# Optimization experiments

Hardware: AMD Instinct MI355X
Metric: run time of the kernel (lower is better)

## Reference

```python
import jax, jax.numpy as jnp
import numpy as np

N_NODES = 100000
N_EDGES = 1600000
IN_CH = 128
HID = 64
N_CLASSES = 16
N_GRAPHS = 64


def setup_inputs() -> dict:
    key = jax.random.key(0)
    ks = jax.random.split(key, 10)
    x = jax.random.normal(ks[0], (N_NODES, IN_CH), dtype=jnp.float32)
    edge_index = jax.random.randint(ks[1], (2, N_EDGES), 0, N_NODES, dtype=jnp.int64)
    edge_weight = jax.random.uniform(ks[2], (N_EDGES,), dtype=jnp.float32)
    batch = jnp.sort(jax.random.randint(ks[3], (N_NODES,), 0, N_GRAPHS, dtype=jnp.int64))
    s1 = 1.0 / np.sqrt(IN_CH)
    s2 = 1.0 / np.sqrt(HID)
    W1 = jax.random.uniform(ks[4], (IN_CH, HID), jnp.float32, -s1, s1)
    b1 = jnp.zeros((HID,), jnp.float32)
    W2 = jax.random.uniform(ks[5], (HID, HID), jnp.float32, -s2, s2)
    b2 = jnp.zeros((HID,), jnp.float32)
    Wl = jax.random.uniform(ks[6], (HID, N_CLASSES), jnp.float32, -s2, s2)
    bl = jax.random.uniform(ks[7], (N_CLASSES,), jnp.float32, -s2, s2)
    return {"x": x, "edge_index": edge_index, "edge_weight": edge_weight,
            "batch": batch, "W1": W1, "b1": b1, "W2": W2, "b2": b2,
            "Wl": Wl, "bl": bl}


def _gcn_conv(x, src, dst, ew, W, b, n_nodes):
    # PyG GCNConv: h = x @ W; symmetric normalization with self-loops;
    # out[dst] += norm * h[src]; out += bias.
    deg = jax.ops.segment_sum(ew, dst, num_segments=n_nodes)
    deg_inv_sqrt = jnp.where(deg > 0, jax.lax.rsqrt(jnp.maximum(deg, 1e-30)), 0.0)
    norm = deg_inv_sqrt[src] * ew * deg_inv_sqrt[dst]  # [E']
    h = x @ W                                          # [N, out]
    msg = h[src] * norm[:, None]                       # [E', out] gather
    out = jax.ops.segment_sum(msg, dst, num_segments=n_nodes)  # scatter-add
    return out + b


def reference(x, edge_index, edge_weight, batch, W1, b1, W2, b2, Wl, bl):
    n = x.shape[0]
    # add self loops once (weight 1.0), shared by both conv layers
    loop = jnp.arange(n, dtype=edge_index.dtype)
    src = jnp.concatenate([edge_index[0], loop])
    dst = jnp.concatenate([edge_index[1], loop])
    ew = jnp.concatenate([edge_weight, jnp.ones((n,), edge_weight.dtype)])

    h = jax.nn.relu(_gcn_conv(x, src, dst, ew, W1, b1, n))
    h = jax.nn.relu(_gcn_conv(h, src, dst, ew, W2, b2, n))

    # global_mean_pool over graphs
    sums = jax.ops.segment_sum(h, batch, num_segments=N_GRAPHS)  # [G, HID]
    cnt = jax.ops.segment_sum(jnp.ones((n,), h.dtype), batch, num_segments=N_GRAPHS)
    pooled = sums / jnp.maximum(cnt, 1.0)[:, None]

    return pooled @ Wl + bl
```

## Files before the change

### kernel.cpp

```cpp
#include <hip/hip_runtime.h>
#include <hip/hip_fp16.h>

#define N_NODES   100000
#define N_EDGES   1600000
#define IN_CH     128
#define HID       64
#define N_CLASSES 16
#define N_GRAPHS  64

#define BK_SH     9
#define BK_NODES  512
#define NB        ((N_NODES + BK_NODES - 1) / BK_NODES)
#define BK_CAP    10240
#define CH_EDGES  4096
#define EPT       16
#define NCH       ((N_EDGES + CH_EDGES - 1) / CH_EDGES)
#define AGG_NPW   2

typedef __attribute__((ext_vector_type(8))) short bf16x8;
typedef __attribute__((ext_vector_type(4))) float f32x4;
typedef __attribute__((ext_vector_type(4))) unsigned u32x4;
typedef __attribute__((ext_vector_type(2))) unsigned u32x2;

__device__ __forceinline__ unsigned short f2bf(float f) {
    unsigned u = __float_as_uint(f);
    u += 0x7fffu + ((u >> 16) & 1u);
    return (unsigned short)(u >> 16);
}
__device__ __forceinline__ f32x4 bf4v(uint2 v) {
    u32x4 u;
    u.x = v.x << 16; u.y = v.x & 0xffff0000u;
    u.z = v.y << 16; u.w = v.y & 0xffff0000u;
    return __builtin_bit_cast(f32x4, u);
}
__device__ __forceinline__ float dec_ew(unsigned v) {
    return __half2float(__ushort_as_half((unsigned short)(v >> 17)));
}

#if __has_builtin(__builtin_amdgcn_make_buffer_rsrc) && \
    __has_builtin(__builtin_amdgcn_raw_buffer_load_b32) && \
    __has_builtin(__builtin_amdgcn_raw_buffer_load_b64)
struct BufView {
    __amdgpu_buffer_rsrc_t rsrc;
    __device__ __forceinline__ void init(const void* p) {
        rsrc = __builtin_amdgcn_make_buffer_rsrc((void*)p, (short)0,
                                                 (int)0xFFFFFFFF, 0x00020000);
    }
    __device__ __forceinline__ unsigned ld32(unsigned off) const {
        return __builtin_amdgcn_raw_buffer_load_b32(rsrc, (int)off, 0, 0);
    }
    __device__ __forceinline__ uint2 ld64(unsigned off) const {
        u32x2 r = __builtin_amdgcn_raw_buffer_load_b64(rsrc, (int)off, 0, 0);
        return make_uint2(r.x, r.y);
    }
};
#else
struct BufView {
    const char* base;
    __device__ __forceinline__ void init(const void* p) { base = (const char*)p; }
    __device__ __forceinline__ unsigned ld32(unsigned off) const {
        return *(const unsigned*)(base + off);
    }
    __device__ __forceinline__ uint2 ld64(unsigned off) const {
        return *(const uint2*)(base + off);
    }
};
#endif

__global__ void k_init(int* __restrict__ bcursor, float* __restrict__ pooled) {
    int i = blockIdx.x * 256 + threadIdx.x;
    if (i < NB) bcursor[i] = i * BK_CAP;
    if (i < N_GRAPHS * HID) pooled[i] = 0.0f;
}

__global__ void k_binscatter(const int* __restrict__ src, const int* __restrict__ dst,
                             const float* __restrict__ ew, int* __restrict__ bcursor,
                             int2* __restrict__ bedges) {
    __shared__ int  hist[NB];
    __shared__ int  offs[NB];
    __shared__ int  gbase[NB];
    __shared__ int  sc[256];
    __shared__ int2 stage[CH_EDGES];
    __shared__ int  dest[CH_EDGES];
    const int t = threadIdx.x;
    const int base = blockIdx.x * CH_EDGES;
    const int nloc = min(CH_EDGES, N_EDGES - base);

    for (int i = t; i < NB; i += 256) hist[i] = 0;
    __syncthreads();

    int myb[EPT], myr[EPT], myp[EPT]; float myw[EPT];
#pragma unroll
    for (int j = 0; j < EPT; ++j) {
        int i = base + j * 256 + t;
        if (i < N_EDGES) {
            int s = src[i], d = dst[i];
            int b = d >> BK_SH;
            myb[j] = b;
            myr[j] = atomicAdd(&hist[b], 1);
            myp[j] = s | ((d & (BK_NODES - 1)) << 17);
            myw[j] = ew[i];
        } else {
            myb[j] = -1;
        }
    }
    __syncthreads();

    int v = (t < NB) ? hist[t] : 0;
    sc[t] = v;
    __syncthreads();
    for (int off = 1; off < 256; off <<= 1) {
        int a = (t >= off) ? sc[t - off] : 0;
        __syncthreads();
        sc[t] += a;
        __syncthreads();
    }
    if (t < NB) {
        offs[t] = sc[t] - v;
        gbase[t] = (v > 0) ? atomicAdd(&bcursor[t], v) : 0;
    }
    __syncthreads();

#pragma unroll
    for (int j = 0; j < EPT; ++j) {
        if (myb[j] >= 0) {
            int p = offs[myb[j]] + myr[j];
            stage[p] = make_int2(myp[j], __float_as_int(myw[j]));
            dest[p] = gbase[myb[j]] + myr[j];
        }
    }
    __syncthreads();

    for (int i = t; i < nloc; i += 256)
        bedges[dest[i]] = stage[i];
}

__global__ __launch_bounds__(256) void k_build(const int* __restrict__ bcursor,
                                               const int2* __restrict__ bedges,
                                               int2* __restrict__ rowse,
                                               float* __restrict__ dis,
                                               unsigned* __restrict__ csr) {
    __shared__ int2  eds[BK_CAP];
    __shared__ int   cnt[BK_NODES];
    __shared__ float dsum[BK_NODES];
    __shared__ int   cur[BK_NODES];
    __shared__ int   sc[256];
    const int b = blockIdx.x;
    const int t = threadIdx.x;
    const int beg = b * BK_CAP, end = bcursor[b];
    const int n = end - beg;

    for (int i = t; i < BK_NODES; i += 256) { cnt[i] = 0; dsum[i] = 0.0f; }
    __syncthreads();

    for (int i = t; i < n; i += 256) {
        int2 e = bedges[beg + i];
        eds[i] = e;
        int dl = ((unsigned)e.x) >> 17;
        atomicAdd(&cnt[dl], 1);
        atomicAdd(&dsum[dl], __int_as_float(e.y));
    }
    __syncthreads();

    int a0 = cnt[2 * t], a1 = cnt[2 * t + 1];
    int pair = a0 + a1;
    sc[t] = pair;
    __syncthreads();
    for (int off = 1; off < 256; off <<= 1) {
        int a = (t >= off) ? sc[t - off] : 0;
        __syncthreads();
        sc[t] += a;
        __syncthreads();
    }
    int excl = sc[t] - pair;
    cur[2 * t] = excl;
    cur[2 * t + 1] = excl + a0;
    {
        int n0 = b * BK_NODES + 2 * t;
        if (n0 < N_NODES) {
            rowse[n0] = make_int2(beg + excl, beg + excl + a0);
            dis[n0] = rsqrtf(1.0f + dsum[2 * t]);
        }
        int n1 = n0 + 1;
        if (n1 < N_NODES) {
            rowse[n1] = make_int2(beg + excl + a0, beg + excl + a0 + a1);
            dis[n1] = rsqrtf(1.0f + dsum[2 * t + 1]);
        }
    }
    __syncthreads();

    for (int i = t; i < n; i += 256) {
        int2 e = eds[i];
        int dl = ((unsigned)e.x) >> 17;
        int s = e.x & 0x1FFFF;
        unsigned short w16 = __half_as_ushort(__float2half(__int_as_float(e.y)));
        int pos = beg + atomicAdd(&cur[dl], 1);
        csr[pos] = (unsigned)s | ((unsigned)w16 << 17);
    }
}

template <int K, bool INB>
__global__ __launch_bounds__(256) void k_gemm(const float* __restrict__ x,
                                              const unsigned short* __restrict__ xb,
                                              const float* __restrict__ W,
                                              const float* __restrict__ dis,
                                              unsigned short* __restrict__ hb) {
    constexpr int AS = K + 8;
    __shared__ unsigned short wt[64 * AS];
    const int t    = threadIdx.x;
    const int lane = t & 63;
    const int wave = t >> 6;
    const int m    = lane & 15;
    const int quad = lane >> 4;
    const int rowbase = blockIdx.x * 64;

    bf16x8 afrag[K / 32];

    if constexpr (!INB) {
        __shared__ unsigned short a_s[64 * AS];
        constexpr int CPR = K / 8;
        for (int c = t; c < 64 * CPR; c += 256) {
            int row = c / CPR, cc = c % CPR;
            int gr = rowbase + row;
            float4 v0, v1;
            if (gr < N_NODES) {
                v0 = *(const float4*)&x[(long)gr * K + cc * 8];
                v1 = *(const float4*)&x[(long)gr * K + cc * 8 + 4];
            } else {
                v0 = make_float4(0.f, 0.f, 0.f, 0.f); v1 = v0;
            }
            uint4 p;
            p.x = f2bf(v0.x) | ((unsigned)f2bf(v0.y) << 16);
            p.y = f2bf(v0.z) | ((unsigned)f2bf(v0.w) << 16);
            p.z = f2bf(v1.x) | ((unsigned)f2bf(v1.y) << 16);
            p.w = f2bf(v1.z) | ((unsigned)f2bf(v1.w) << 16);
            *(uint4*)&a_s[row * AS + cc * 8] = p;
        }
        for (int idx = t; idx < K * 64; idx += 256) {
            int k = idx >> 6, n = idx & 63;
            wt[n * AS + k] = f2bf(W[idx]);
        }
        __syncthreads();
#pragma unroll
        for (int ks = 0; ks < K / 32; ++ks)
            afrag[ks] = *(const bf16x8*)&a_s[(wave * 16 + m) * AS + ks * 32 + quad * 8];
    } else {
        const int gr = rowbase + wave * 16 + m;
#pragma unroll
        for (int ks = 0; ks < K / 32; ++ks) {
            if (gr < N_NODES)
                afrag[ks] = *(const bf16x8*)&xb[(long)gr * K + ks * 32 + quad * 8];
            else
                afrag[ks] = (bf16x8){0, 0, 0, 0, 0, 0, 0, 0};
        }
        for (int idx = t; idx < K * 64; idx += 256) {
            int k = idx >> 6, n = idx & 63;
            wt[n * AS + k] = f2bf(W[idx]);
        }
        __syncthreads();
    }

    bf16x8 bfrag[4][K / 32];
#pragma unroll
    for (int nt = 0; nt < 4; ++nt)
#pragma unroll
        for (int ks = 0; ks < K / 32; ++ks)
            bfrag[nt][ks] = *(const bf16x8*)&wt[(nt * 16 + m) * AS + ks * 32 + quad * 8];

    f32x4 acc[4];
#pragma unroll
    for (int nt = 0; nt < 4; ++nt) acc[nt] = (f32x4){0.f, 0.f, 0.f, 0.f};

#pragma unroll
    for (int ks = 0; ks < K / 32; ++ks) {
#pragma unroll
        for (int nt = 0; nt < 4; ++nt)
            acc[nt] = __builtin_amdgcn_mfma_f32_16x16x32_bf16(afrag[ks], bfrag[nt][ks],
                                                              acc[nt], 0, 0, 0);
    }

#pragma unroll
    for (int i = 0; i < 4; ++i) {
        int gr = rowbase + wave * 16 + quad * 4 + i;
        if (gr < N_NODES) {
            float dsc = dis[gr];
#pragma unroll
            for (int nt = 0; nt < 4; ++nt)
                hb[(long)gr * HID + nt * 16 + m] = f2bf(dsc * acc[nt][i]);
        }
    }
}

#define NEXTBLK(pb_, eb_, jb_, hv_)                                           \
    do {                                                                      \
        if (p0 < e0)      { pb_ = p0; eb_ = e0; jb_ = 0; hv_ = true; p0 += 16; } \
        else if (p1 < e1) { pb_ = p1; eb_ = e1; jb_ = 1; hv_ = true; p1 += 16; } \
        else              { hv_ = false; }                                    \
    } while (0)

#define AGG_STEP(pC_, eC_, jC_, c0_, c1_, c2_, c3_, r0_, r1_, r2_, r3_, hC_,  \
                 n0_, n1_, n2_, n3_, s0_, s1_, s2_, s3_, hN_)                 \
    do {                                                                      \
        const float w0_ = (pC_ + g      < eC_) ? dec_ew(c0_) : 0.f;           \
        const float w1_ = (pC_ + 4 + g  < eC_) ? dec_ew(c1_) : 0.f;           \
        const float w2_ = (pC_ + 8 + g  < eC_) ? dec_ew(c2_) : 0.f;           \
        const float w3_ = (pC_ + 12 + g < eC_) ? dec_ew(c3_) : 0.f;           \
        const int jcur_ = jC_;                                                \
        if (hN_) {        \
            s0_ = vh.ld64(((n0_ & 0x1FFFF) << 7) | coff);                     \
            s1_ = vh.ld64(((n1_ & 0x1FFFF) << 7) | coff);                     \
            s2_ = vh.ld64(((n2_ & 0x1FFFF) << 7) | coff);                     \
            s3_ = vh.ld64(((n3_ & 0x1FFFF) << 7) | coff);                     \
        }                                                                     \
        NEXTBLK(pC_, eC_, jC_, hC_);    \
        if (hC_) {                                                            \
            const int last_ = eC_ - 1;                                        \
            c0_ = vc.ld32((unsigned)(min(pC_ + g,      last_) << 2));         \
            c1_ = vc.ld32((unsigned)(min(pC_ + 4 + g,  last_) << 2));         \
            c2_ = vc.ld32((unsigned)(min(pC_ + 8 + g,  last_) << 2));         \
            c3_ = vc.ld32((unsigned)(min(pC_ + 12 + g, last_) << 2));         \
        }                                                                     \
        f32x4 t_ = bf4v(r0_) * w0_;                                           \
        t_ += bf4v(r1_) * w1_;                                                \
        t_ += bf4v(r2_) * w2_;                                                \
        t_ += bf4v(r3_) * w3_;                                                \
        if (jcur_ == 0) acc0 += t_; else acc1 += t_;                          \
    } while (0)

template <bool OB>
__global__ __launch_bounds__(256) void k_aggregate(const int2* __restrict__ rowse,
                            const unsigned* __restrict__ csr,
                            const uint2* __restrict__ hb, const float* __restrict__ dis,
                            const float* __restrict__ b, const int* __restrict__ batch,
                            float* __restrict__ pooled, uint2* __restrict__ outb) {
    __shared__ float psh[4 * AGG_NPW][HID];
    const int tid  = threadIdx.x;
    const int lane = tid & 63;
    const int g    = lane >> 4;
    const int c4   = lane & 15;
    const int wave = tid >> 6;
    const int node0 = (blockIdx.x * 4 + wave) * AGG_NPW;
    const float4 bb = ((const float4*)b)[c4];
    const f32x4 bbv = {bb.x, bb.y, bb.z, bb.w};

    BufView vc; vc.init(csr);
    BufView vh; vh.init(hb);
    const unsigned coff = (unsigned)(c4 << 3);

    const int2 rs0 = rowse[node0];
    const int2 rs1 = rowse[node0 + 1];
    const uint2 hs0 = hb[node0 * 16 + c4];
    const uint2 hs1 = hb[(node0 + 1) * 16 + c4];
    const float dd0 = dis[node0];
    const float dd1 = dis[node0 + 1];

    f32x4 acc0 = (g == 0) ? bf4v(hs0) : (f32x4){0.f, 0.f, 0.f, 0.f};
    f32x4 acc1 = (g == 0) ? bf4v(hs1) : (f32x4){0.f, 0.f, 0.f, 0.f};

    int p0 = rs0.x, e0 = rs0.y, p1 = rs1.x, e1 = rs1.y;

    int pA = 0, eAn = 0, jA = 0; bool hA = false;
    int pB = 0, eBn = 0, jB = 0; bool hB = false;
    unsigned cA0 = 0, cA1 = 0, cA2 = 0, cA3 = 0;
    unsigned cB0 = 0, cB1 = 0, cB2 = 0, cB3 = 0;
    uint2 rA0 = {0, 0}, rA1 = {0, 0}, rA2 = {0, 0}, rA3 = {0, 0};
    uint2 rB0 = {0, 0}, rB1 = {0, 0}, rB2 = {0, 0}, rB3 = {0, 0};

    NEXTBLK(pA, eAn, jA, hA);
    if (hA) {
        const int last = eAn - 1;
        cA0 = vc.ld32((unsigned)(min(pA + g,      last) << 2));
        cA1 = vc.ld32((unsigned)(min(pA + 4 + g,  last) << 2));
        cA2 = vc.ld32((unsigned)(min(pA + 8 + g,  last) << 2));
        cA3 = vc.ld32((unsigned)(min(pA + 12 + g, last) << 2));
        NEXTBLK(pB, eBn, jB, hB);
        if (hB) {
            const int lastB = eBn - 1;
            cB0 = vc.ld32((unsigned)(min(pB + g,      lastB) << 2));
            cB1 = vc.ld32((unsigned)(min(pB + 4 + g,  lastB) << 2));
            cB2 = vc.ld32((unsigned)(min(pB + 8 + g,  lastB) << 2));
            cB3 = vc.ld32((unsigned)(min(pB + 12 + g, lastB) << 2));
        }
        rA0 = vh.ld64(((cA0 & 0x1FFFF) << 7) | coff);
        rA1 = vh.ld64(((cA1 & 0x1FFFF) << 7) | coff);
        rA2 = vh.ld64(((cA2 & 0x1FFFF) << 7) | coff);
        rA3 = vh.ld64(((cA3 & 0x1FFFF) << 7) | coff);
    }

    bool par = false;
    while (par ? hB : hA) {
        if (!par) {
            AGG_STEP(pA, eAn, jA, cA0, cA1, cA2, cA3, rA0, rA1, rA2, rA3, hA,
                     cB0, cB1, cB2, cB3, rB0, rB1, rB2, rB3, hB);
        } else {
            AGG_STEP(pB, eBn, jB, cB0, cB1, cB2, cB3, rB0, rB1, rB2, rB3, hB,
                     cA0, cA1, cA2, cA3, rA0, rA1, rA2, rA3, hA);
        }
        par = !par;
    }

#pragma unroll
    for (int i = 0; i < 4; ++i) {
        float t0 = acc0[i];
        t0 += __shfl_xor(t0, 16); t0 += __shfl_xor(t0, 32);
        acc0[i] = t0;
        float t1 = acc1[i];
        t1 += __shfl_xor(t1, 16); t1 += __shfl_xor(t1, 32);
        acc1[i] = t1;
    }

    if (g == 0) {
        f32x4 o0 = acc0 * dd0 + bbv;
        f32x4 o1 = acc1 * dd1 + bbv;
        o0.x = fmaxf(o0.x, 0.f); o0.y = fmaxf(o0.y, 0.f);
        o0.z = fmaxf(o0.z, 0.f); o0.w = fmaxf(o0.w, 0.f);
        o1.x = fmaxf(o1.x, 0.f); o1.y = fmaxf(o1.y, 0.f);
        o1.z = fmaxf(o1.z, 0.f); o1.w = fmaxf(o1.w, 0.f);
        if constexpr (OB) {
            uint2 pk0, pk1;
            pk0.x = (unsigned)f2bf(o0.x) | ((unsigned)f2bf(o0.y) << 16);
            pk0.y = (unsigned)f2bf(o0.z) | ((unsigned)f2bf(o0.w) << 16);
            pk1.x = (unsigned)f2bf(o1.x) | ((unsigned)f2bf(o1.y) << 16);
            pk1.y = (unsigned)f2bf(o1.z) | ((unsigned)f2bf(o1.w) << 16);
            outb[node0 * 16 + c4] = pk0;
            outb[(node0 + 1) * 16 + c4] = pk1;
        } else {
            *(f32x4*)&psh[wave * AGG_NPW][c4 * 4] = o0;
            *(f32x4*)&psh[wave * AGG_NPW + 1][c4 * 4] = o1;
        }
    }

    if constexpr (!OB) {
        __syncthreads();
        if (tid < HID) {
            const int nb0 = blockIdx.x * 4 * AGG_NPW;
            int curg = batch[nb0];
            float a = 0.f;
#pragma unroll
            for (int j = 0; j < 4 * AGG_NPW; ++j) {
                int bg = batch[nb0 + j];
                if (bg != curg) {
                    atomicAdd(&pooled[curg * HID + tid], a);
                    a = 0.f; curg = bg;
                }
                a += psh[j][tid];
            }
            atomicAdd(&pooled[curg * HID + tid], a);
        }
    }
}

__global__ __launch_bounds__(1024) void k_out(const float* __restrict__ pooled,
                      const int* __restrict__ batch,
                      const float* __restrict__ Wl, const float* __restrict__ bl,
                      float* __restrict__ out) {
    __shared__ int bnd[N_GRAPHS + 1];
    int tid = threadIdx.x;
    if (tid <= N_GRAPHS) {
        int target = tid;
        int lo = 0, hi = N_NODES;
        while (lo < hi) {
            int mid = (lo + hi) >> 1;
            if (batch[mid] < target) lo = mid + 1; else hi = mid;
        }
        bnd[tid] = lo;
    }
    __syncthreads();
    int g = tid >> 4, k = tid & 15;
    float cntg = (float)(bnd[g + 1] - bnd[g]);
    float inv = 1.0f / fmaxf(cntg, 1.0f);
    float acc = 0.f;
#pragma unroll
    for (int h = 0; h < HID; ++h) acc += pooled[g * HID + h] * Wl[h * N_CLASSES + k];
    out[g * N_CLASSES + k] = acc * inv + bl[k];
}

extern "C" void kernel_launch(void* const* d_in, const int* in_sizes, int n_in,
                              void* d_out, int out_size, void* d_ws, size_t ws_size,
                              hipStream_t stream) {
    const float* x     = (const float*)d_in[0];
    const int*   ei    = (const int*)d_in[1];
    const float* ew    = (const float*)d_in[2];
    const int*   batch = (const int*)d_in[3];
    const float* W1    = (const float*)d_in[4];
    const float* b1    = (const float*)d_in[5];
    const float* W2    = (const float*)d_in[6];
    const float* b2    = (const float*)d_in[7];
    const float* Wl    = (const float*)d_in[8];
    const float* bl    = (const float*)d_in[9];

    const int* srcv = ei;
    const int* dstv = ei + N_EDGES;

    char* wsb = (char*)d_ws;
    float*          dis    = (float*)wsb;              wsb += 100352 * 4;
    int2*           rowse  = (int2*)wsb;               wsb += 100352 * 8;
    int*            bcursor= (int*)wsb;                wsb += 256 * 4;
    unsigned*       csr    = (unsigned*)wsb;           wsb += (size_t)NB * BK_CAP * 4;
    unsigned short* hb     = (unsigned short*)wsb;     wsb += N_NODES * HID * 2;
    char*           scratch= wsb;                      wsb += N_NODES * HID * 4;
    float*          pooled = (float*)wsb;              wsb += N_GRAPHS * HID * 4;
    float*          out    = (float*)d_out;
    int2*           bedges = (int2*)scratch;
    unsigned short* hbA    = (unsigned short*)scratch;

    k_init<<<16, 256, 0, stream>>>(bcursor, pooled);
    k_binscatter<<<NCH, 256, 0, stream>>>(srcv, dstv, ew, bcursor, bedges);
    k_build<<<NB, 256, 0, stream>>>(bcursor, bedges, rowse, dis, csr);

    const int agg_blocks = (N_NODES + 4 * AGG_NPW - 1) / (4 * AGG_NPW);

    k_gemm<IN_CH, false><<<(N_NODES + 63) / 64, 256, 0, stream>>>(x, nullptr, W1, dis, hb);
    k_aggregate<true><<<agg_blocks, 256, 0, stream>>>(rowse, csr, (const uint2*)hb,
                                                      dis, b1, batch, nullptr, (uint2*)hbA);
    k_gemm<HID, true><<<(N_NODES + 63) / 64, 256, 0, stream>>>(nullptr, hbA, W2, dis, hb);
    k_aggregate<false><<<agg_blocks, 256, 0, stream>>>(rowse, csr, (const uint2*)hb,
                                                       dis, b2, batch, pooled, nullptr);

    k_out<<<1, 1024, 0, stream>>>(pooled, batch, Wl, bl, out);
}
```

Before: 274.7 us.

## Restructure aggregation loop into interleaved full-block fast path plus masked tail

The two-node aggregation loop, which used ping-pong software pipelining with per-step block selection and masked weights, is replaced by a loop that interleaves full 16-edge blocks for both nodes without bounds masking. The partial tail block is handled once with clamped indices. Row ranges are read with a single int4 load, the dis loads move to the epilogue, and launch_bounds is dropped. This cuts per-step branching and masking overhead but loses the explicit prefetch of the next block's gathered rows, which may expose more memory latency.

```diff
diff --git a/kernel.cpp b/kernel.cpp
--- a/kernel.cpp
+++ b/kernel.cpp
@@ -291,44 +291,29 @@
     }
 }
 
-#define NEXTBLK(pb_, eb_, jb_, hv_)                                           \
+
+#define FULLBLK(pX, eX, f_, x0, x1, x2, x3, accX)                             \
     do {                                                                      \
-        if (p0 < e0)      { pb_ = p0; eb_ = e0; jb_ = 0; hv_ = true; p0 += 16; } \
-        else if (p1 < e1) { pb_ = p1; eb_ = e1; jb_ = 1; hv_ = true; p1 += 16; } \
-        else              { hv_ = false; }                                    \
+        const unsigned e0_ = x0, e1_ = x1, e2_ = x2, e3_ = x3;                \
+        pX += 16;                                                             \
+        f_ = (pX + 16 <= eX);                                                 \
+        if (f_) {                                                             \
+            const unsigned v_ = (unsigned)((pX + g) << 2);                    \
+            x0 = vc.ld32(v_);      x1 = vc.ld32(v_ + 16);                     \
+            x2 = vc.ld32(v_ + 32); x3 = vc.ld32(v_ + 48);                     \
+        }                                                                     \
+        f32x4 v0_ = bf4v(vh.ld64(((e0_ & 0x1FFFF) << 7) | coff));             \
+        f32x4 v1_ = bf4v(vh.ld64(((e1_ & 0x1FFFF) << 7) | coff));             \
+        f32x4 v2_ = bf4v(vh.ld64(((e2_ & 0x1FFFF) << 7) | coff));             \
+        f32x4 v3_ = bf4v(vh.ld64(((e3_ & 0x1FFFF) << 7) | coff));             \
+        accX += v0_ * dec_ew(e0_);                                            \
+        accX += v1_ * dec_ew(e1_);                                            \
+        accX += v2_ * dec_ew(e2_);                                            \
+        accX += v3_ * dec_ew(e3_);                                            \
     } while (0)
 
-#define AGG_STEP(pC_, eC_, jC_, c0_, c1_, c2_, c3_, r0_, r1_, r2_, r3_, hC_,  \
-                 n0_, n1_, n2_, n3_, s0_, s1_, s2_, s3_, hN_)                 \
-    do {                                                                      \
-        const float w0_ = (pC_ + g      < eC_) ? dec_ew(c0_) : 0.f;           \
-        const float w1_ = (pC_ + 4 + g  < eC_) ? dec_ew(c1_) : 0.f;           \
-        const float w2_ = (pC_ + 8 + g  < eC_) ? dec_ew(c2_) : 0.f;           \
-        const float w3_ = (pC_ + 12 + g < eC_) ? dec_ew(c3_) : 0.f;           \
-        const int jcur_ = jC_;                                                \
-        if (hN_) {        \
-            s0_ = vh.ld64(((n0_ & 0x1FFFF) << 7) | coff);                     \
-            s1_ = vh.ld64(((n1_ & 0x1FFFF) << 7) | coff);                     \
-            s2_ = vh.ld64(((n2_ & 0x1FFFF) << 7) | coff);                     \
-            s3_ = vh.ld64(((n3_ & 0x1FFFF) << 7) | coff);                     \
-        }                                                                     \
-        NEXTBLK(pC_, eC_, jC_, hC_);    \
-        if (hC_) {                                                            \
-            const int last_ = eC_ - 1;                                        \
-            c0_ = vc.ld32((unsigned)(min(pC_ + g,      last_) << 2));         \
-            c1_ = vc.ld32((unsigned)(min(pC_ + 4 + g,  last_) << 2));         \
-            c2_ = vc.ld32((unsigned)(min(pC_ + 8 + g,  last_) << 2));         \
-            c3_ = vc.ld32((unsigned)(min(pC_ + 12 + g, last_) << 2));         \
-        }                                                                     \
-        f32x4 t_ = bf4v(r0_) * w0_;                                           \
-        t_ += bf4v(r1_) * w1_;                                                \
-        t_ += bf4v(r2_) * w2_;                                                \
-        t_ += bf4v(r3_) * w3_;                                                \
-        if (jcur_ == 0) acc0 += t_; else acc1 += t_;                          \
-    } while (0)
-
 template <bool OB>
-__global__ __launch_bounds__(256) void k_aggregate(const int2* __restrict__ rowse,
+__global__ void k_aggregate(const int2* __restrict__ rowse,
                             const unsigned* __restrict__ csr,
                             const uint2* __restrict__ hb, const float* __restrict__ dis,
                             const float* __restrict__ b, const int* __restrict__ batch,
@@ -340,6 +325,7 @@
     const int c4   = lane & 15;
     const int wave = tid >> 6;
     const int node0 = (blockIdx.x * 4 + wave) * AGG_NPW;
+    const int node1 = node0 + 1;
     const float4 bb = ((const float4*)b)[c4];
     const f32x4 bbv = {bb.x, bb.y, bb.z, bb.w};
 
@@ -347,56 +333,75 @@
     BufView vh; vh.init(hb);
     const unsigned coff = (unsigned)(c4 << 3);
 
-    const int2 rs0 = rowse[node0];
-    const int2 rs1 = rowse[node0 + 1];
+    const int4 rr = *(const int4*)&rowse[node0];
     const uint2 hs0 = hb[node0 * 16 + c4];
-    const uint2 hs1 = hb[(node0 + 1) * 16 + c4];
-    const float dd0 = dis[node0];
-    const float dd1 = dis[node0 + 1];
+    const uint2 hs1 = hb[node1 * 16 + c4];
 
     f32x4 acc0 = (g == 0) ? bf4v(hs0) : (f32x4){0.f, 0.f, 0.f, 0.f};
     f32x4 acc1 = (g == 0) ? bf4v(hs1) : (f32x4){0.f, 0.f, 0.f, 0.f};
 
-    int p0 = rs0.x, e0 = rs0.y, p1 = rs1.x, e1 = rs1.y;
-
-    int pA = 0, eAn = 0, jA = 0; bool hA = false;
-    int pB = 0, eBn = 0, jB = 0; bool hB = false;
-    unsigned cA0 = 0, cA1 = 0, cA2 = 0, cA3 = 0;
-    unsigned cB0 = 0, cB1 = 0, cB2 = 0, cB3 = 0;
-    uint2 rA0 = {0, 0}, rA1 = {0, 0}, rA2 = {0, 0}, rA3 = {0, 0};
-    uint2 rB0 = {0, 0}, rB1 = {0, 0}, rB2 = {0, 0}, rB3 = {0, 0};
-
-    NEXTBLK(pA, eAn, jA, hA);
-    if (hA) {
-        const int last = eAn - 1;
-        cA0 = vc.ld32((unsigned)(min(pA + g,      last) << 2));
-        cA1 = vc.ld32((unsigned)(min(pA + 4 + g,  last) << 2));
-        cA2 = vc.ld32((unsigned)(min(pA + 8 + g,  last) << 2));
-        cA3 = vc.ld32((unsigned)(min(pA + 12 + g, last) << 2));
-        NEXTBLK(pB, eBn, jB, hB);
-        if (hB) {
-            const int lastB = eBn - 1;
-            cB0 = vc.ld32((unsigned)(min(pB + g,      lastB) << 2));
-            cB1 = vc.ld32((unsigned)(min(pB + 4 + g,  lastB) << 2));
-            cB2 = vc.ld32((unsigned)(min(pB + 8 + g,  lastB) << 2));
-            cB3 = vc.ld32((unsigned)(min(pB + 12 + g, lastB) << 2));
-        }
-        rA0 = vh.ld64(((cA0 & 0x1FFFF) << 7) | coff);
-        rA1 = vh.ld64(((cA1 & 0x1FFFF) << 7) | coff);
-        rA2 = vh.ld64(((cA2 & 0x1FFFF) << 7) | coff);
-        rA3 = vh.ld64(((cA3 & 0x1FFFF) << 7) | coff);
-    }
-
-    bool par = false;
-    while (par ? hB : hA) {
-        if (!par) {
-            AGG_STEP(pA, eAn, jA, cA0, cA1, cA2, cA3, rA0, rA1, rA2, rA3, hA,
-                     cB0, cB1, cB2, cB3, rB0, rB1, rB2, rB3, hB);
-        } else {
-            AGG_STEP(pB, eBn, jB, cB0, cB1, cB2, cB3, rB0, rB1, rB2, rB3, hB,
-                     cA0, cA1, cA2, cA3, rA0, rA1, rA2, rA3, hA);
-        }
-        par = !par;
+    int p0 = rr.x; const int e0 = rr.y;
+    int p1 = rr.z; const int e1 = rr.w;
+
+    unsigned a0 = 0, a1 = 0, a2 = 0, a3 = 0;
+    unsigned b0 = 0, b1 = 0, b2 = 0, b3 = 0;
+    bool fA = (p0 + 16 <= e0);
+    bool fB = (p1 + 16 <= e1);
+    if (fA) {
+        const unsigned v = (unsigned)((p0 + g) << 2);
+        a0 = vc.ld32(v);      a1 = vc.ld32(v + 16);
+        a2 = vc.ld32(v + 32); a3 = vc.ld32(v + 48);
+    }
+    if (fB) {
+        const unsigned v = (unsigned)((p1 + g) << 2);
+        b0 = vc.ld32(v);      b1 = vc.ld32(v + 16);
+        b2 = vc.ld32(v + 32); b3 = vc.ld32(v + 48);
+    }
+
+    while (fA && fB) {
+        FULLBLK(p0, e0, fA, a0, a1, a2, a3, acc0);
+        FULLBLK(p1, e1, fB, b0, b1, b2, b3, acc1);
+    }
+    while (fA) FULLBLK(p0, e0, fA, a0, a1, a2, a3, acc0);
+    while (fB) FULLBLK(p1, e1, fB, b0, b1, b2, b3, acc1);
+
+    const bool tA = (p0 < e0);
+    const bool tB = (p1 < e1);
+    unsigned ta0 = 0, ta1 = 0, ta2 = 0, ta3 = 0;
+    unsigned tb0 = 0, tb1 = 0, tb2 = 0, tb3 = 0;
+    if (tA) {
+        const int last = e0 - 1;
+        ta0 = vc.ld32((unsigned)(min(p0 + g,      last) << 2));
+        ta1 = vc.ld32((unsigned)(min(p0 + 4 + g,  last) << 2));
+        ta2 = vc.ld32((unsigned)(min(p0 + 8 + g,  last) << 2));
+        ta3 = vc.ld32((unsigned)(min(p0 + 12 + g, last) << 2));
+    }
+    if (tB) {
+        const int last = e1 - 1;
+        tb0 = vc.ld32((unsigned)(min(p1 + g,      last) << 2));
+        tb1 = vc.ld32((unsigned)(min(p1 + 4 + g,  last) << 2));
+        tb2 = vc.ld32((unsigned)(min(p1 + 8 + g,  last) << 2));
+        tb3 = vc.ld32((unsigned)(min(p1 + 12 + g, last) << 2));
+    }
+    if (tA) {
+        f32x4 v0 = bf4v(vh.ld64(((ta0 & 0x1FFFF) << 7) | coff));
+        f32x4 v1 = bf4v(vh.ld64(((ta1 & 0x1FFFF) << 7) | coff));
+        f32x4 v2 = bf4v(vh.ld64(((ta2 & 0x1FFFF) << 7) | coff));
+        f32x4 v3 = bf4v(vh.ld64(((ta3 & 0x1FFFF) << 7) | coff));
+        acc0 += v0 * ((p0 + g      < e0) ? dec_ew(ta0) : 0.f);
+        acc0 += v1 * ((p0 + 4 + g  < e0) ? dec_ew(ta1) : 0.f);
+        acc0 += v2 * ((p0 + 8 + g  < e0) ? dec_ew(ta2) : 0.f);
+        acc0 += v3 * ((p0 + 12 + g < e0) ? dec_ew(ta3) : 0.f);
+    }
+    if (tB) {
+        f32x4 v0 = bf4v(vh.ld64(((tb0 & 0x1FFFF) << 7) | coff));
+        f32x4 v1 = bf4v(vh.ld64(((tb1 & 0x1FFFF) << 7) | coff));
+        f32x4 v2 = bf4v(vh.ld64(((tb2 & 0x1FFFF) << 7) | coff));
+        f32x4 v3 = bf4v(vh.ld64(((tb3 & 0x1FFFF) << 7) | coff));
+        acc1 += v0 * ((p1 + g      < e1) ? dec_ew(tb0) : 0.f);
+        acc1 += v1 * ((p1 + 4 + g  < e1) ? dec_ew(tb1) : 0.f);
+        acc1 += v2 * ((p1 + 8 + g  < e1) ? dec_ew(tb2) : 0.f);
+        acc1 += v3 * ((p1 + 12 + g < e1) ? dec_ew(tb3) : 0.f);
     }
 
 #pragma unroll
@@ -410,6 +415,8 @@
     }
 
     if (g == 0) {
+        const float dd0 = dis[node0];
+        const float dd1 = dis[node1];
         f32x4 o0 = acc0 * dd0 + bbv;
         f32x4 o1 = acc1 * dd1 + bbv;
         o0.x = fmaxf(o0.x, 0.f); o0.y = fmaxf(o0.y, 0.f);
@@ -423,7 +430,7 @@
             pk1.x = (unsigned)f2bf(o1.x) | ((unsigned)f2bf(o1.y) << 16);
             pk1.y = (unsigned)f2bf(o1.z) | ((unsigned)f2bf(o1.w) << 16);
             outb[node0 * 16 + c4] = pk0;
-            outb[(node0 + 1) * 16 + c4] = pk1;
+            outb[node1 * 16 + c4] = pk1;
         } else {
             *(f32x4*)&psh[wave * AGG_NPW][c4 * 4] = o0;
             *(f32x4*)&psh[wave * AGG_NPW + 1][c4 * 4] = o1;
@@ -508,7 +515,7 @@
     k_binscatter<<<NCH, 256, 0, stream>>>(srcv, dstv, ew, bcursor, bedges);
     k_build<<<NB, 256, 0, stream>>>(bcursor, bedges, rowse, dis, csr);
 
-    const int agg_blocks = (N_NODES + 4 * AGG_NPW - 1) / (4 * AGG_NPW);
+    const int agg_blocks = N_NODES / (4 * AGG_NPW);
 
     k_gemm<IN_CH, false><<<(N_NODES + 63) / 64, 256, 0, stream>>>(x, nullptr, W1, dis, hb);
     k_aggregate<true><<<agg_blocks, 256, 0, stream>>>(rowse, csr, (const uint2*)hb,
```

Measured after the change: 255.8 us. 6.9% less time.
